# Optimization experiments

Hardware: AMD Instinct MI355X
Metric: run time of the kernel (lower is better)

Reference implementation:

```python
import jax, jax.numpy as jnp
import numpy as np

L, D, F, V = 24, 1024, 4096, 50277  # n_layer, n_embd, ffn hidden (4*D), vocab
RESCALE = 6


def _ln(x, w, b, eps=1e-5):
    m = jnp.mean(x, axis=-1, keepdims=True)
    v = jnp.mean(jnp.square(x - m), axis=-1, keepdims=True)
    return (x - m) * jax.lax.rsqrt(v + eps) * w + b


def setup_inputs() -> dict:
    key = jax.random.key(0)
    ks = iter(jax.random.split(key, 64))

    def nrm(shape, s=0.02):
        return jax.random.normal(next(ks), shape, jnp.float32) * s

    def uni(shape):
        return jax.random.uniform(next(ks), shape, jnp.float32)

    state = jnp.zeros((L, 5, D), jnp.float32).at[:, 4, :].set(-1e30)  # pp init
    return {
        "token_embd": jax.random.normal(next(ks), (D,), jnp.float32),
        "state": state,
        "emb_ln_w": jnp.ones((D,), jnp.float32),
        "emb_ln_b": jnp.zeros((D,), jnp.float32),
        "ln1_w": jnp.ones((L, D), jnp.float32),
        "ln1_b": jnp.zeros((L, D), jnp.float32),
        "ln2_w": jnp.ones((L, D), jnp.float32),
        "ln2_b": jnp.zeros((L, D), jnp.float32),
        "att_tmk": uni((L, D)),
        "att_tmv": uni((L, D)),
        "att_tmr": uni((L, D)),
        "att_tf": nrm((L, D), 0.5),
        "att_td": -jnp.exp(nrm((L, D), 0.5)),  # time_decay = -exp(w) at load
        "att_kw": nrm((L, D, D)),
        "att_vw": nrm((L, D, D)),
        "att_rw": nrm((L, D, D)),
        "att_ow": nrm((L, D, D)),
        "ffn_tmk": uni((L, D)),
        "ffn_tmr": uni((L, D)),
        "ffn_kw": nrm((L, F, D)),
        "ffn_vw": nrm((L, D, F)),
        "ffn_rw": nrm((L, D, D)),
        "out_ln_w": jnp.ones((D,), jnp.float32),
        "out_ln_b": jnp.zeros((D,), jnp.float32),
        "head_w": nrm((V, D)),
    }


def reference(token_embd, state, emb_ln_w, emb_ln_b, ln1_w, ln1_b, ln2_w, ln2_b,
              att_tmk, att_tmv, att_tmr, att_tf, att_td, att_kw, att_vw, att_rw,
              att_ow, ffn_tmk, ffn_tmr, ffn_kw, ffn_vw, ffn_rw,
              out_ln_w, out_ln_b, head_w):
    x0 = _ln(token_embd, emb_ln_w, emb_ln_b)  # encoder

    def layer(x, inputs):
        (i, st, l1w, l1b, l2w, l2b, tmk, tmv, tmr, tf, td,
         kw, vw, rw, ow, ftmk, ftmr, fkw, fvw, frw) = inputs
        # ---- time mixing ----
        xn = _ln(x, l1w, l1b)
        s_att, aa, bb, pp = st[1], st[2], st[3], st[4]
        xk = xn * tmk + s_att * (1 - tmk)
        xv = xn * tmv + s_att * (1 - tmv)
        xr = xn * tmr + s_att * (1 - tmr)
        r = jax.nn.sigmoid(rw @ xr)
        kk = kw @ xk
        vv = vw @ xv
        ww = tf + kk
        p = jnp.maximum(pp, ww)
        e1 = jnp.exp(pp - p)
        e2 = jnp.exp(ww - p)
        a = e1 * aa + e2 * vv
        b = e1 * bb + e2
        ww2 = pp + td
        p2 = jnp.maximum(ww2, kk)
        f1 = jnp.exp(ww2 - p2)
        f2 = jnp.exp(kk - p2)
        new_aa = f1 * aa + f2 * vv
        new_bb = f1 * bb + f2
        x = x + ow @ (r * (a / b))
        # ---- channel mixing ----
        xn2 = _ln(x, l2w, l2b)
        s_ffn = st[0]
        xk2 = xn2 * ftmk + s_ffn * (1 - ftmk)
        xr2 = xn2 * ftmr + s_ffn * (1 - ftmr)
        r2 = jax.nn.sigmoid(frw @ xr2)
        k2 = jnp.square(jax.nn.relu(fkw @ xk2))
        x = x + r2 * (fvw @ k2)
        # rescale every RESCALE layers
        x = jnp.where((i + 1) % RESCALE == 0, x * 0.5, x)
        new_st = jnp.stack([xn2, xn, new_aa, new_bb, p2])
        return x, new_st

    idx = jnp.arange(L)
    x, new_state = jax.lax.scan(
        layer, x0,
        (idx, state, ln1_w, ln1_b, ln2_w, ln2_b, att_tmk, att_tmv, att_tmr,
         att_tf, att_td, att_kw, att_vw, att_rw, att_ow, ffn_tmk, ffn_tmr,
         ffn_kw, ffn_vw, ffn_rw))
    logits = head_w @ _ln(x, out_ln_w, out_ln_b)  # decoder
    return logits, new_state
```

## Files before the change

### kernel.cpp

```cpp
#include <hip/hip_runtime.h>

#define DD 1024
#define FF 4096
#define LL 24
#define VV 50277


__device__ __forceinline__ float wave_sum(float v) {
#pragma unroll
    for (int o = 32; o > 0; o >>= 1) v += __shfl_xor(v, o, 64);
    return v;
}

__device__ __forceinline__ float block_sum(float v, float* scr) {
    v = wave_sum(v);
    int w = threadIdx.x >> 6;
    __syncthreads();
    if ((threadIdx.x & 63) == 0) scr[w] = v;
    __syncthreads();
    return scr[0] + scr[1] + scr[2] + scr[3];
}

__device__ __forceinline__ float4 ln_vec(float4 xv, const float* __restrict__ w,
                                         const float* __restrict__ b,
                                         float* scr, int t) {
    float s = xv.x + xv.y + xv.z + xv.w;
    float m = block_sum(s, scr) * (1.0f / (float)DD);
    float dx = xv.x - m, dy = xv.y - m, dz = xv.z - m, dw = xv.w - m;
    float var = block_sum(dx * dx + dy * dy + dz * dz + dw * dw, scr) * (1.0f / (float)DD);
    float rs = rsqrtf(var + 1e-5f);
    float4 w4 = ((const float4*)w)[t];
    float4 b4 = ((const float4*)b)[t];
    return make_float4(dx * rs * w4.x + b4.x, dy * rs * w4.y + b4.y,
                       dz * rs * w4.z + b4.z, dw * rs * w4.w + b4.w);
}


__global__ __launch_bounds__(256) void k_ln(const float* __restrict__ xin,
                                            const float* __restrict__ w,
                                            const float* __restrict__ b,
                                            float* __restrict__ xout) {
    __shared__ float scr[4];
    int t = threadIdx.x;
    float4 v = ((const float4*)xin)[t];
    float4 n = ln_vec(v, w, b, scr, t);
    ((float4*)xout)[t] = n;
}


__global__ __launch_bounds__(256) void k1_timemix(
    const float* __restrict__ x, const float* __restrict__ st,
    const float* __restrict__ l1w, const float* __restrict__ l1b,
    const float* __restrict__ tmk, const float* __restrict__ tmv,
    const float* __restrict__ tmr,
    const float* __restrict__ kw, const float* __restrict__ vw,
    const float* __restrict__ rw,
    float* __restrict__ kk, float* __restrict__ vv, float* __restrict__ rr,
    float* __restrict__ st_out) {
    __shared__ __align__(16) float xk[DD];
    __shared__ __align__(16) float xv_[DD];
    __shared__ __align__(16) float xr[DD];
    __shared__ float scr[4];
    int t = threadIdx.x;

    float4 xvec = ((const float4*)x)[t];
    float4 n = ln_vec(xvec, l1w, l1b, scr, t);
    if (blockIdx.x == 0) ((float4*)(st_out + DD))[t] = n;

    float4 sa = ((const float4*)(st + DD))[t];
    float4 mk = ((const float4*)tmk)[t];
    float4 mv = ((const float4*)tmv)[t];
    float4 mr = ((const float4*)tmr)[t];
    ((float4*)xk)[t] = make_float4(n.x * mk.x + sa.x * (1.f - mk.x),
                                   n.y * mk.y + sa.y * (1.f - mk.y),
                                   n.z * mk.z + sa.z * (1.f - mk.z),
                                   n.w * mk.w + sa.w * (1.f - mk.w));
    ((float4*)xv_)[t] = make_float4(n.x * mv.x + sa.x * (1.f - mv.x),
                                    n.y * mv.y + sa.y * (1.f - mv.y),
                                    n.z * mv.z + sa.z * (1.f - mv.z),
                                    n.w * mv.w + sa.w * (1.f - mv.w));
    ((float4*)xr)[t] = make_float4(n.x * mr.x + sa.x * (1.f - mr.x),
                                   n.y * mr.y + sa.y * (1.f - mr.y),
                                   n.z * mr.z + sa.z * (1.f - mr.z),
                                   n.w * mr.w + sa.w * (1.f - mr.w));
    __syncthreads();

    int lane = t & 63, w = t >> 6;
    int ridx = blockIdx.x * 4 + w;
    int m = ridx >> 10, row = ridx & 1023;
    const float* W = (m == 0 ? kw : (m == 1 ? vw : rw)) + (size_t)row * DD;
    const float* vec = (m == 0 ? xk : (m == 1 ? xv_ : xr));
    const float4* W4 = (const float4*)W;
    const float4* v4 = (const float4*)vec;
    float acc = 0.f;
#pragma unroll
    for (int j = 0; j < 4; ++j) {
        float4 a = W4[lane + 64 * j];
        float4 bx = v4[lane + 64 * j];
        acc = fmaf(a.x, bx.x, fmaf(a.y, bx.y, fmaf(a.z, bx.z, fmaf(a.w, bx.w, acc))));
    }
    acc = wave_sum(acc);
    if (lane == 0) {
        if (m == 0) kk[row] = acc;
        else if (m == 1) vv[row] = acc;
        else rr[row] = 1.0f / (1.0f + expf(-acc));
    }
}


__global__ __launch_bounds__(256) void k2_wkv_out(
    const float* __restrict__ st,
    const float* __restrict__ tf, const float* __restrict__ td,
    const float* __restrict__ kk, const float* __restrict__ vv,
    const float* __restrict__ rr, const float* __restrict__ ow,
    float* __restrict__ x, float* __restrict__ st_out) {
    __shared__ __align__(16) float rab[DD];
    int t = threadIdx.x;

    float4 kk4 = ((const float4*)kk)[t];
    float4 vv4 = ((const float4*)vv)[t];
    float4 r4  = ((const float4*)rr)[t];
    float4 aa4 = ((const float4*)(st + 2 * DD))[t];
    float4 bb4 = ((const float4*)(st + 3 * DD))[t];
    float4 pp4 = ((const float4*)(st + 4 * DD))[t];
    float4 tf4 = ((const float4*)tf)[t];
    float4 td4 = ((const float4*)td)[t];
    float4 rabv, naa, nbb, np2;
    const float* kkp = (const float*)&kk4; const float* vvp = (const float*)&vv4;
    const float* rp = (const float*)&r4;   const float* aap = (const float*)&aa4;
    const float* bbp = (const float*)&bb4; const float* ppp = (const float*)&pp4;
    const float* tfp = (const float*)&tf4; const float* tdp = (const float*)&td4;
#pragma unroll
    for (int c = 0; c < 4; ++c) {
        float kx = kkp[c], vx = vvp[c], rx = rp[c];
        float ax = aap[c], bx = bbp[c], px = ppp[c];
        float ww = tfp[c] + kx;
        float p = fmaxf(px, ww);
        float e1 = expf(px - p), e2 = expf(ww - p);
        float a = e1 * ax + e2 * vx;
        float b = e1 * bx + e2;
        ((float*)&rabv)[c] = rx * (a / b);
        float ww2 = px + tdp[c];
        float p2 = fmaxf(ww2, kx);
        float f1 = expf(ww2 - p2), f2 = expf(kx - p2);
        ((float*)&naa)[c] = f1 * ax + f2 * vx;
        ((float*)&nbb)[c] = f1 * bx + f2;
        ((float*)&np2)[c] = p2;
    }
    ((float4*)rab)[t] = rabv;
    if (blockIdx.x == 0) {
        ((float4*)(st_out + 2 * DD))[t] = naa;
        ((float4*)(st_out + 3 * DD))[t] = nbb;
        ((float4*)(st_out + 4 * DD))[t] = np2;
    }
    __syncthreads();

    int lane = t & 63, w = t >> 6;
    int row = blockIdx.x * 4 + w;
    const float4* W4 = (const float4*)(ow + (size_t)row * DD);
    const float4* v4 = (const float4*)rab;
    float acc = 0.f;
#pragma unroll
    for (int j = 0; j < 4; ++j) {
        float4 a = W4[lane + 64 * j];
        float4 bx = v4[lane + 64 * j];
        acc = fmaf(a.x, bx.x, fmaf(a.y, bx.y, fmaf(a.z, bx.z, fmaf(a.w, bx.w, acc))));
    }
    acc = wave_sum(acc);
    if (lane == 0) x[row] += acc;
}


__global__ __launch_bounds__(256) void k3_ffn_kr(
    const float* __restrict__ x, const float* __restrict__ st,
    const float* __restrict__ l2w, const float* __restrict__ l2b,
    const float* __restrict__ ftmk, const float* __restrict__ ftmr,
    const float* __restrict__ fkw, const float* __restrict__ frw,
    float* __restrict__ k2, float* __restrict__ r2, float* __restrict__ st_out) {
    __shared__ __align__(16) float xk2[DD];
    __shared__ __align__(16) float xr2[DD];
    __shared__ float scr[4];
    int t = threadIdx.x;

    float4 xvec = ((const float4*)x)[t];
    float4 n = ln_vec(xvec, l2w, l2b, scr, t);
    if (blockIdx.x == 0) ((float4*)st_out)[t] = n;

    float4 sf = ((const float4*)st)[t];
    float4 mk = ((const float4*)ftmk)[t];
    float4 mr = ((const float4*)ftmr)[t];
    ((float4*)xk2)[t] = make_float4(n.x * mk.x + sf.x * (1.f - mk.x),
                                    n.y * mk.y + sf.y * (1.f - mk.y),
                                    n.z * mk.z + sf.z * (1.f - mk.z),
                                    n.w * mk.w + sf.w * (1.f - mk.w));
    ((float4*)xr2)[t] = make_float4(n.x * mr.x + sf.x * (1.f - mr.x),
                                    n.y * mr.y + sf.y * (1.f - mr.y),
                                    n.z * mr.z + sf.z * (1.f - mr.z),
                                    n.w * mr.w + sf.w * (1.f - mr.w));
    __syncthreads();

    int lane = t & 63, w = t >> 6;
    int ridx = blockIdx.x * 4 + w;
    const float* W;
    const float* vec;
    if (ridx < FF) { W = fkw + (size_t)ridx * DD; vec = xk2; }
    else           { W = frw + (size_t)(ridx - FF) * DD; vec = xr2; }
    const float4* W4 = (const float4*)W;
    const float4* v4 = (const float4*)vec;
    float acc = 0.f;
#pragma unroll
    for (int j = 0; j < 4; ++j) {
        float4 a = W4[lane + 64 * j];
        float4 bx = v4[lane + 64 * j];
        acc = fmaf(a.x, bx.x, fmaf(a.y, bx.y, fmaf(a.z, bx.z, fmaf(a.w, bx.w, acc))));
    }
    acc = wave_sum(acc);
    if (lane == 0) {
        if (ridx < FF) {
            float rl = fmaxf(acc, 0.f);
            k2[ridx] = rl * rl;
        } else {
            r2[ridx - FF] = 1.0f / (1.0f + expf(-acc));
        }
    }
}


__global__ __launch_bounds__(256) void k4_ffn_v(
    const float* __restrict__ fvw, const float* __restrict__ k2,
    const float* __restrict__ r2, float* __restrict__ x, float scale) {
    __shared__ __align__(16) float k2s[FF];
    int t = threadIdx.x;
#pragma unroll
    for (int j = 0; j < 4; ++j)
        ((float4*)k2s)[t + 256 * j] = ((const float4*)k2)[t + 256 * j];
    __syncthreads();

    int lane = t & 63, w = t >> 6;
    int row = blockIdx.x * 4 + w;
    const float4* W4 = (const float4*)(fvw + (size_t)row * FF);
    const float4* v4 = (const float4*)k2s;
    float acc = 0.f;
#pragma unroll
    for (int j = 0; j < 16; ++j) {
        float4 a = W4[lane + 64 * j];
        float4 bx = v4[lane + 64 * j];
        acc = fmaf(a.x, bx.x, fmaf(a.y, bx.y, fmaf(a.z, bx.z, fmaf(a.w, bx.w, acc))));
    }
    acc = wave_sum(acc);
    if (lane == 0) x[row] = (x[row] + r2[row] * acc) * scale;
}


__global__ __launch_bounds__(256) void k_head(const float* __restrict__ head_w,
                                              const float* __restrict__ xn,
                                              float* __restrict__ logits) {
    __shared__ __align__(16) float xs[DD];
    int t = threadIdx.x;
    ((float4*)xs)[t] = ((const float4*)xn)[t];
    __syncthreads();

    int lane = t & 63, w = t >> 6;
    int row = blockIdx.x * 4 + w;
    if (row >= VV) return;
    const float4* W4 = (const float4*)(head_w + (size_t)row * DD);
    const float4* v4 = (const float4*)xs;
    float acc = 0.f;
#pragma unroll
    for (int j = 0; j < 4; ++j) {
        float4 a = W4[lane + 64 * j];
        float4 bx = v4[lane + 64 * j];
        acc = fmaf(a.x, bx.x, fmaf(a.y, bx.y, fmaf(a.z, bx.z, fmaf(a.w, bx.w, acc))));
    }
    acc = wave_sum(acc);
    if (lane == 0) logits[row] = acc;
}


extern "C" void kernel_launch(void* const* d_in, const int* in_sizes, int n_in,
                              void* d_out, int out_size, void* d_ws, size_t ws_size,
                              hipStream_t stream) {
    const float* token_embd = (const float*)d_in[0];
    const float* state      = (const float*)d_in[1];
    const float* emb_ln_w   = (const float*)d_in[2];
    const float* emb_ln_b   = (const float*)d_in[3];
    const float* ln1_w      = (const float*)d_in[4];
    const float* ln1_b      = (const float*)d_in[5];
    const float* ln2_w      = (const float*)d_in[6];
    const float* ln2_b      = (const float*)d_in[7];
    const float* att_tmk    = (const float*)d_in[8];
    const float* att_tmv    = (const float*)d_in[9];
    const float* att_tmr    = (const float*)d_in[10];
    const float* att_tf     = (const float*)d_in[11];
    const float* att_td     = (const float*)d_in[12];
    const float* att_kw     = (const float*)d_in[13];
    const float* att_vw     = (const float*)d_in[14];
    const float* att_rw     = (const float*)d_in[15];
    const float* att_ow     = (const float*)d_in[16];
    const float* ffn_tmk    = (const float*)d_in[17];
    const float* ffn_tmr    = (const float*)d_in[18];
    const float* ffn_kw     = (const float*)d_in[19];
    const float* ffn_vw     = (const float*)d_in[20];
    const float* ffn_rw     = (const float*)d_in[21];
    const float* out_ln_w   = (const float*)d_in[22];
    const float* out_ln_b   = (const float*)d_in[23];
    const float* head_w     = (const float*)d_in[24];

    float* logits = (float*)d_out;
    float* st_out_base = (float*)d_out + VV;

    float* ws  = (float*)d_ws;
    float* x   = ws;
    float* kk  = ws + 1024;
    float* vv  = ws + 2048;
    float* rr  = ws + 3072;
    float* k2  = ws + 4096;
    float* r2  = ws + 8192;
    float* xnH = ws + 9216;

    k_ln<<<1, 256, 0, stream>>>(token_embd, emb_ln_w, emb_ln_b, x);

    for (int i = 0; i < LL; ++i) {
        const float* st = state + (size_t)i * 5 * DD;
        float* sto = st_out_base + (size_t)i * 5 * DD;
        k1_timemix<<<768, 256, 0, stream>>>(
            x, st, ln1_w + i * DD, ln1_b + i * DD,
            att_tmk + i * DD, att_tmv + i * DD, att_tmr + i * DD,
            att_kw + (size_t)i * DD * DD, att_vw + (size_t)i * DD * DD,
            att_rw + (size_t)i * DD * DD, kk, vv, rr, sto);
        k2_wkv_out<<<256, 256, 0, stream>>>(
            st, att_tf + i * DD, att_td + i * DD, kk, vv, rr,
            att_ow + (size_t)i * DD * DD, x, sto);
        k3_ffn_kr<<<1280, 256, 0, stream>>>(
            x, st, ln2_w + i * DD, ln2_b + i * DD,
            ffn_tmk + i * DD, ffn_tmr + i * DD,
            ffn_kw + (size_t)i * FF * DD, ffn_rw + (size_t)i * DD * DD,
            k2, r2, sto);
        float scale = ((i + 1) % 6 == 0) ? 0.5f : 1.0f;
        k4_ffn_v<<<256, 256, 0, stream>>>(
            ffn_vw + (size_t)i * DD * FF, k2, r2, x, scale);
    }

    k_ln<<<1, 256, 0, stream>>>(x, out_ln_w, out_ln_b, xnH);
    k_head<<<(VV + 3) / 4, 256, 0, stream>>>(head_w, xnH, logits);
}
```

Baseline: 610.2 us.

## Prefetch upcoming layer weights into cache via extra blocks in each kernel

Each per-layer kernel gets PFB extra blocks that stream the weights needed by the next kernels (attention output, FFN key/value/receptance, next layer's k/v/r) through the cache, so that later GEMVs hit in cache (likely the large MI355X last-level cache) instead of HBM. The encoder layernorm is fused into the first time-mix kernel and the output layernorm into the head kernel, removing two single-block launches. Head rows are loaded before the layernorm to overlap latency. This relies on cache capacity and adds redundant memory traffic that competes with the current kernel's own loads.

```diff
diff --git a/kernel.cpp b/kernel.cpp
--- a/kernel.cpp
+++ b/kernel.cpp
@@ -4,6 +4,9 @@
 #define FF 4096
 #define LL 24
 #define VV 50277
+#define PFB 256
+
+typedef float v4f __attribute__((ext_vector_type(4)));
 
 
 __device__ __forceinline__ float wave_sum(float v) {
@@ -21,152 +24,150 @@
     return scr[0] + scr[1] + scr[2] + scr[3];
 }
 
-__device__ __forceinline__ float4 ln_vec(float4 xv, const float* __restrict__ w,
-                                         const float* __restrict__ b,
-                                         float* scr, int t) {
-    float s = xv.x + xv.y + xv.z + xv.w;
-    float m = block_sum(s, scr) * (1.0f / (float)DD);
-    float dx = xv.x - m, dy = xv.y - m, dz = xv.z - m, dw = xv.w - m;
-    float var = block_sum(dx * dx + dy * dy + dz * dz + dw * dw, scr) * (1.0f / (float)DD);
+__device__ __forceinline__ v4f ln_vec(v4f xv, const float* __restrict__ w,
+                                      const float* __restrict__ b, float* scr, int t) {
+    float m = block_sum(xv[0] + xv[1] + xv[2] + xv[3], scr) * (1.0f / 1024.0f);
+    v4f d = xv - m;
+    float var = block_sum(d[0]*d[0] + d[1]*d[1] + d[2]*d[2] + d[3]*d[3], scr) * (1.0f / 1024.0f);
     float rs = rsqrtf(var + 1e-5f);
-    float4 w4 = ((const float4*)w)[t];
-    float4 b4 = ((const float4*)b)[t];
-    return make_float4(dx * rs * w4.x + b4.x, dy * rs * w4.y + b4.y,
-                       dz * rs * w4.z + b4.z, dw * rs * w4.w + b4.w);
-}
-
-
-__global__ __launch_bounds__(256) void k_ln(const float* __restrict__ xin,
-                                            const float* __restrict__ w,
-                                            const float* __restrict__ b,
-                                            float* __restrict__ xout) {
-    __shared__ float scr[4];
-    int t = threadIdx.x;
-    float4 v = ((const float4*)xin)[t];
-    float4 n = ln_vec(v, w, b, scr, t);
-    ((float4*)xout)[t] = n;
+    v4f w4 = ((const v4f*)w)[t], b4 = ((const v4f*)b)[t];
+    return d * rs * w4 + b4;
+}
+
+__device__ __forceinline__ v4f mixv(v4f n, v4f s, v4f m) { return n * m + s * (1.0f - m); }
+
+__device__ __forceinline__ float dotv(v4f a, v4f x) {
+    return fmaf(a[0], x[0], fmaf(a[1], x[1], fmaf(a[2], x[2], a[3] * x[3])));
+}
+
+struct Row { v4f a, b, c, d; };
+
+__device__ __forceinline__ void row_load(Row& r, const float* p, int lane) {
+    const v4f* q = (const v4f*)p;
+    r.a = q[lane]; r.b = q[lane + 64]; r.c = q[lane + 128]; r.d = q[lane + 192];
+}
+__device__ __forceinline__ float row_dot(const Row& r, const v4f* v, int lane) {
+    return dotv(r.a, v[lane]) + dotv(r.b, v[lane + 64]) +
+           dotv(r.c, v[lane + 128]) + dotv(r.d, v[lane + 192]);
+}
+
+
+__device__ __forceinline__ void pf_region(const float* p, int nvec, int pb, int t) {
+    if (p == nullptr || nvec <= 0) return;
+    const v4f* q = (const v4f*)p;
+    int chunk = (nvec + PFB - 1) / PFB;
+    int lo = pb * chunk;
+    int end = lo + chunk; if (end > nvec) end = nvec;
+    int i = lo + t;
+    v4f a0 = {0,0,0,0}, a1 = a0, a2 = a0, a3 = a0, a4 = a0, a5 = a0, a6 = a0, a7 = a0;
+    for (; i + 1792 < end; i += 2048) {
+        v4f t0 = q[i],        t1 = q[i + 256],  t2 = q[i + 512],  t3 = q[i + 768];
+        v4f t4 = q[i + 1024], t5 = q[i + 1280], t6 = q[i + 1536], t7 = q[i + 1792];
+        a0 += t0; a1 += t1; a2 += t2; a3 += t3;
+        a4 += t4; a5 += t5; a6 += t6; a7 += t7;
+    }
+    for (; i < end; i += 256) a0 += q[i];
+    a0 = (a0 + a1) + (a2 + a3) + ((a4 + a5) + (a6 + a7));
+    asm volatile("" :: "v"(a0));
 }
 
 
 __global__ __launch_bounds__(256) void k1_timemix(
-    const float* __restrict__ x, const float* __restrict__ st,
+    const float* __restrict__ xin, const float* __restrict__ st,
+    const float* __restrict__ enc_w, const float* __restrict__ enc_b,
     const float* __restrict__ l1w, const float* __restrict__ l1b,
     const float* __restrict__ tmk, const float* __restrict__ tmv,
     const float* __restrict__ tmr,
     const float* __restrict__ kw, const float* __restrict__ vw,
     const float* __restrict__ rw,
     float* __restrict__ kk, float* __restrict__ vv, float* __restrict__ rr,
-    float* __restrict__ st_out) {
-    __shared__ __align__(16) float xk[DD];
-    __shared__ __align__(16) float xv_[DD];
-    __shared__ __align__(16) float xr[DD];
+    float* __restrict__ x0out, float* __restrict__ st_out,
+    const float* pfa, int na, const float* pfb, int nb) {
+    const int t = threadIdx.x;
+    int b = blockIdx.x;
+    if (b < PFB) { pf_region(pfa, na, b, t); pf_region(pfb, nb, b, t); return; }
+    b -= PFB;
+    __shared__ __align__(16) float s_k[DD], s_v[DD], s_r[DD];
     __shared__ float scr[4];
-    int t = threadIdx.x;
-
-    float4 xvec = ((const float4*)x)[t];
-    float4 n = ln_vec(xvec, l1w, l1b, scr, t);
-    if (blockIdx.x == 0) ((float4*)(st_out + DD))[t] = n;
-
-    float4 sa = ((const float4*)(st + DD))[t];
-    float4 mk = ((const float4*)tmk)[t];
-    float4 mv = ((const float4*)tmv)[t];
-    float4 mr = ((const float4*)tmr)[t];
-    ((float4*)xk)[t] = make_float4(n.x * mk.x + sa.x * (1.f - mk.x),
-                                   n.y * mk.y + sa.y * (1.f - mk.y),
-                                   n.z * mk.z + sa.z * (1.f - mk.z),
-                                   n.w * mk.w + sa.w * (1.f - mk.w));
-    ((float4*)xv_)[t] = make_float4(n.x * mv.x + sa.x * (1.f - mv.x),
-                                    n.y * mv.y + sa.y * (1.f - mv.y),
-                                    n.z * mv.z + sa.z * (1.f - mv.z),
-                                    n.w * mv.w + sa.w * (1.f - mv.w));
-    ((float4*)xr)[t] = make_float4(n.x * mr.x + sa.x * (1.f - mr.x),
-                                   n.y * mr.y + sa.y * (1.f - mr.y),
-                                   n.z * mr.z + sa.z * (1.f - mr.z),
-                                   n.w * mr.w + sa.w * (1.f - mr.w));
-    __syncthreads();
-
-    int lane = t & 63, w = t >> 6;
-    int ridx = blockIdx.x * 4 + w;
-    int m = ridx >> 10, row = ridx & 1023;
-    const float* W = (m == 0 ? kw : (m == 1 ? vw : rw)) + (size_t)row * DD;
-    const float* vec = (m == 0 ? xk : (m == 1 ? xv_ : xr));
-    const float4* W4 = (const float4*)W;
-    const float4* v4 = (const float4*)vec;
-    float acc = 0.f;
-#pragma unroll
-    for (int j = 0; j < 4; ++j) {
-        float4 a = W4[lane + 64 * j];
-        float4 bx = v4[lane + 64 * j];
-        acc = fmaf(a.x, bx.x, fmaf(a.y, bx.y, fmaf(a.z, bx.z, fmaf(a.w, bx.w, acc))));
-    }
-    acc = wave_sum(acc);
+    const int lane = t & 63, w = t >> 6;
+
+    v4f xv = ((const v4f*)xin)[t];
+    if (enc_w) xv = ln_vec(xv, enc_w, enc_b, scr, t);
+    if (x0out && b == 0) ((v4f*)x0out)[t] = xv;
+    v4f n = ln_vec(xv, l1w, l1b, scr, t);
+    if (b == 0) ((v4f*)(st_out + DD))[t] = n;
+    {
+        v4f sa = ((const v4f*)(st + DD))[t];
+        ((v4f*)s_k)[t] = mixv(n, sa, ((const v4f*)tmk)[t]);
+        ((v4f*)s_v)[t] = mixv(n, sa, ((const v4f*)tmv)[t]);
+        ((v4f*)s_r)[t] = mixv(n, sa, ((const v4f*)tmr)[t]);
+    }
+    __syncthreads();
+
+    const int ridx = b * 4 + w, m = ridx >> 10, row = ridx & 1023;
+    Row W;
+    row_load(W, (m == 0 ? kw : m == 1 ? vw : rw) + (size_t)row * DD, lane);
+    const v4f* vec = (const v4f*)(m == 0 ? s_k : m == 1 ? s_v : s_r);
+    float acc = wave_sum(row_dot(W, vec, lane));
     if (lane == 0) {
-        if (m == 0) kk[row] = acc;
+        if (m == 0)      kk[row] = acc;
         else if (m == 1) vv[row] = acc;
-        else rr[row] = 1.0f / (1.0f + expf(-acc));
+        else             rr[row] = 1.0f / (1.0f + expf(-acc));
     }
 }
 
 
 __global__ __launch_bounds__(256) void k2_wkv_out(
-    const float* __restrict__ st,
-    const float* __restrict__ tf, const float* __restrict__ td,
+    const float* __restrict__ st, const float* __restrict__ tf,
+    const float* __restrict__ td,
     const float* __restrict__ kk, const float* __restrict__ vv,
     const float* __restrict__ rr, const float* __restrict__ ow,
-    float* __restrict__ x, float* __restrict__ st_out) {
+    float* __restrict__ x, float* __restrict__ st_out,
+    const float* pfa, int na, const float* pfb, int nb) {
+    const int t = threadIdx.x;
+    int b = blockIdx.x;
+    if (b < PFB) { pf_region(pfa, na, b, t); pf_region(pfb, nb, b, t); return; }
+    b -= PFB;
     __shared__ __align__(16) float rab[DD];
-    int t = threadIdx.x;
-
-    float4 kk4 = ((const float4*)kk)[t];
-    float4 vv4 = ((const float4*)vv)[t];
-    float4 r4  = ((const float4*)rr)[t];
-    float4 aa4 = ((const float4*)(st + 2 * DD))[t];
-    float4 bb4 = ((const float4*)(st + 3 * DD))[t];
-    float4 pp4 = ((const float4*)(st + 4 * DD))[t];
-    float4 tf4 = ((const float4*)tf)[t];
-    float4 td4 = ((const float4*)td)[t];
-    float4 rabv, naa, nbb, np2;
-    const float* kkp = (const float*)&kk4; const float* vvp = (const float*)&vv4;
-    const float* rp = (const float*)&r4;   const float* aap = (const float*)&aa4;
-    const float* bbp = (const float*)&bb4; const float* ppp = (const float*)&pp4;
-    const float* tfp = (const float*)&tf4; const float* tdp = (const float*)&td4;
+    const int lane = t & 63, w = t >> 6;
+
+    {
+        v4f kx = ((const v4f*)kk)[t];
+        v4f vx = ((const v4f*)vv)[t];
+        v4f rx = ((const v4f*)rr)[t];
+        v4f aa = ((const v4f*)(st + 2 * DD))[t];
+        v4f bb = ((const v4f*)(st + 3 * DD))[t];
+        v4f pp = ((const v4f*)(st + 4 * DD))[t];
+        v4f tf4 = ((const v4f*)tf)[t];
+        v4f td4 = ((const v4f*)td)[t];
+        v4f rb, naa, nbb, np2;
 #pragma unroll
-    for (int c = 0; c < 4; ++c) {
-        float kx = kkp[c], vx = vvp[c], rx = rp[c];
-        float ax = aap[c], bx = bbp[c], px = ppp[c];
-        float ww = tfp[c] + kx;
-        float p = fmaxf(px, ww);
-        float e1 = expf(px - p), e2 = expf(ww - p);
-        float a = e1 * ax + e2 * vx;
-        float b = e1 * bx + e2;
-        ((float*)&rabv)[c] = rx * (a / b);
-        float ww2 = px + tdp[c];
-        float p2 = fmaxf(ww2, kx);
-        float f1 = expf(ww2 - p2), f2 = expf(kx - p2);
-        ((float*)&naa)[c] = f1 * ax + f2 * vx;
-        ((float*)&nbb)[c] = f1 * bx + f2;
-        ((float*)&np2)[c] = p2;
-    }
-    ((float4*)rab)[t] = rabv;
-    if (blockIdx.x == 0) {
-        ((float4*)(st_out + 2 * DD))[t] = naa;
-        ((float4*)(st_out + 3 * DD))[t] = nbb;
-        ((float4*)(st_out + 4 * DD))[t] = np2;
-    }
-    __syncthreads();
-
-    int lane = t & 63, w = t >> 6;
-    int row = blockIdx.x * 4 + w;
-    const float4* W4 = (const float4*)(ow + (size_t)row * DD);
-    const float4* v4 = (const float4*)rab;
-    float acc = 0.f;
-#pragma unroll
-    for (int j = 0; j < 4; ++j) {
-        float4 a = W4[lane + 64 * j];
-        float4 bx = v4[lane + 64 * j];
-        acc = fmaf(a.x, bx.x, fmaf(a.y, bx.y, fmaf(a.z, bx.z, fmaf(a.w, bx.w, acc))));
-    }
-    acc = wave_sum(acc);
+        for (int c = 0; c < 4; ++c) {
+            float kc = kx[c], vc = vx[c];
+            float wwc = tf4[c] + kc;
+            float p = fmaxf(pp[c], wwc);
+            float e1 = expf(pp[c] - p), e2 = expf(wwc - p);
+            rb[c] = rx[c] * ((e1 * aa[c] + e2 * vc) / (e1 * bb[c] + e2));
+            float ww2 = pp[c] + td4[c];
+            float p2 = fmaxf(ww2, kc);
+            float f1 = expf(ww2 - p2), f2 = expf(kc - p2);
+            naa[c] = f1 * aa[c] + f2 * vc;
+            nbb[c] = f1 * bb[c] + f2;
+            np2[c] = p2;
+        }
+        ((v4f*)rab)[t] = rb;
+        if (b == 0) {
+            ((v4f*)(st_out + 2 * DD))[t] = naa;
+            ((v4f*)(st_out + 3 * DD))[t] = nbb;
+            ((v4f*)(st_out + 4 * DD))[t] = np2;
+        }
+    }
+    __syncthreads();
+
+    const int row = b * 4 + w;
+    Row W;
+    row_load(W, ow + (size_t)row * DD, lane);
+    float acc = wave_sum(row_dot(W, (const v4f*)rab, lane));
     if (lane == 0) x[row] += acc;
 }
 
@@ -176,76 +177,65 @@
     const float* __restrict__ l2w, const float* __restrict__ l2b,
     const float* __restrict__ ftmk, const float* __restrict__ ftmr,
     const float* __restrict__ fkw, const float* __restrict__ frw,
-    float* __restrict__ k2, float* __restrict__ r2, float* __restrict__ st_out) {
-    __shared__ __align__(16) float xk2[DD];
-    __shared__ __align__(16) float xr2[DD];
+    float* __restrict__ k2, float* __restrict__ r2, float* __restrict__ st_out,
+    const float* pfa, int na, const float* pfb, int nb) {
+    const int t = threadIdx.x;
+    int b = blockIdx.x;
+    if (b < PFB) { pf_region(pfa, na, b, t); pf_region(pfb, nb, b, t); return; }
+    b -= PFB;
+    __shared__ __align__(16) float s_k[DD], s_r[DD];
     __shared__ float scr[4];
-    int t = threadIdx.x;
-
-    float4 xvec = ((const float4*)x)[t];
-    float4 n = ln_vec(xvec, l2w, l2b, scr, t);
-    if (blockIdx.x == 0) ((float4*)st_out)[t] = n;
-
-    float4 sf = ((const float4*)st)[t];
-    float4 mk = ((const float4*)ftmk)[t];
-    float4 mr = ((const float4*)ftmr)[t];
-    ((float4*)xk2)[t] = make_float4(n.x * mk.x + sf.x * (1.f - mk.x),
-                                    n.y * mk.y + sf.y * (1.f - mk.y),
-                                    n.z * mk.z + sf.z * (1.f - mk.z),
-                                    n.w * mk.w + sf.w * (1.f - mk.w));
-    ((float4*)xr2)[t] = make_float4(n.x * mr.x + sf.x * (1.f - mr.x),
-                                    n.y * mr.y + sf.y * (1.f - mr.y),
-                                    n.z * mr.z + sf.z * (1.f - mr.z),
-                                    n.w * mr.w + sf.w * (1.f - mr.w));
-    __syncthreads();
-
-    int lane = t & 63, w = t >> 6;
-    int ridx = blockIdx.x * 4 + w;
-    const float* W;
-    const float* vec;
-    if (ridx < FF) { W = fkw + (size_t)ridx * DD; vec = xk2; }
-    else           { W = frw + (size_t)(ridx - FF) * DD; vec = xr2; }
-    const float4* W4 = (const float4*)W;
-    const float4* v4 = (const float4*)vec;
-    float acc = 0.f;
-#pragma unroll
-    for (int j = 0; j < 4; ++j) {
-        float4 a = W4[lane + 64 * j];
-        float4 bx = v4[lane + 64 * j];
-        acc = fmaf(a.x, bx.x, fmaf(a.y, bx.y, fmaf(a.z, bx.z, fmaf(a.w, bx.w, acc))));
-    }
-    acc = wave_sum(acc);
+    const int lane = t & 63, w = t >> 6;
+
+    v4f xv = ((const v4f*)x)[t];
+    v4f n = ln_vec(xv, l2w, l2b, scr, t);
+    if (b == 0) ((v4f*)st_out)[t] = n;
+    {
+        v4f sf = ((const v4f*)st)[t];
+        ((v4f*)s_k)[t] = mixv(n, sf, ((const v4f*)ftmk)[t]);
+        ((v4f*)s_r)[t] = mixv(n, sf, ((const v4f*)ftmr)[t]);
+    }
+    __syncthreads();
+
+    const int ridx = b * 4 + w;
+    const float* Wp;
+    const v4f* vec;
+    if (ridx < FF) { Wp = fkw + (size_t)ridx * DD; vec = (const v4f*)s_k; }
+    else           { Wp = frw + (size_t)(ridx - FF) * DD; vec = (const v4f*)s_r; }
+    Row W;
+    row_load(W, Wp, lane);
+    float acc = wave_sum(row_dot(W, vec, lane));
     if (lane == 0) {
-        if (ridx < FF) {
-            float rl = fmaxf(acc, 0.f);
-            k2[ridx] = rl * rl;
-        } else {
-            r2[ridx - FF] = 1.0f / (1.0f + expf(-acc));
-        }
+        if (ridx < FF) { float rl = fmaxf(acc, 0.f); k2[ridx] = rl * rl; }
+        else           r2[ridx - FF] = 1.0f / (1.0f + expf(-acc));
     }
 }
 
 
 __global__ __launch_bounds__(256) void k4_ffn_v(
     const float* __restrict__ fvw, const float* __restrict__ k2,
-    const float* __restrict__ r2, float* __restrict__ x, float scale) {
+    const float* __restrict__ r2, float* __restrict__ x, float scale,
+    const float* pfa, int na, const float* pfb, int nb) {
+    const int t = threadIdx.x;
+    int b = blockIdx.x;
+    if (b < PFB) { pf_region(pfa, na, b, t); pf_region(pfb, nb, b, t); return; }
+    b -= PFB;
     __shared__ __align__(16) float k2s[FF];
-    int t = threadIdx.x;
+    const int lane = t & 63, w = t >> 6;
 #pragma unroll
     for (int j = 0; j < 4; ++j)
-        ((float4*)k2s)[t + 256 * j] = ((const float4*)k2)[t + 256 * j];
-    __syncthreads();
-
-    int lane = t & 63, w = t >> 6;
-    int row = blockIdx.x * 4 + w;
-    const float4* W4 = (const float4*)(fvw + (size_t)row * FF);
-    const float4* v4 = (const float4*)k2s;
+        ((v4f*)k2s)[t + 256 * j] = ((const v4f*)k2)[t + 256 * j];
+    __syncthreads();
+
+    const int row = b * 4 + w;
+    const v4f* W4 = (const v4f*)(fvw + (size_t)row * FF);
+    const v4f* v4 = (const v4f*)k2s;
     float acc = 0.f;
 #pragma unroll
     for (int j = 0; j < 16; ++j) {
-        float4 a = W4[lane + 64 * j];
-        float4 bx = v4[lane + 64 * j];
-        acc = fmaf(a.x, bx.x, fmaf(a.y, bx.y, fmaf(a.z, bx.z, fmaf(a.w, bx.w, acc))));
+        v4f a = W4[lane + 64 * j];
+        v4f bx = v4[lane + 64 * j];
+        acc = fmaf(a[0], bx[0], fmaf(a[1], bx[1], fmaf(a[2], bx[2], fmaf(a[3], bx[3], acc))));
     }
     acc = wave_sum(acc);
     if (lane == 0) x[row] = (x[row] + r2[row] * acc) * scale;
@@ -253,27 +243,24 @@
 
 
 __global__ __launch_bounds__(256) void k_head(const float* __restrict__ head_w,
-                                              const float* __restrict__ xn,
+                                              const float* __restrict__ x,
+                                              const float* __restrict__ olw,
+                                              const float* __restrict__ olb,
                                               float* __restrict__ logits) {
     __shared__ __align__(16) float xs[DD];
-    int t = threadIdx.x;
-    ((float4*)xs)[t] = ((const float4*)xn)[t];
-    __syncthreads();
-
-    int lane = t & 63, w = t >> 6;
-    int row = blockIdx.x * 4 + w;
-    if (row >= VV) return;
-    const float4* W4 = (const float4*)(head_w + (size_t)row * DD);
-    const float4* v4 = (const float4*)xs;
-    float acc = 0.f;
-#pragma unroll
-    for (int j = 0; j < 4; ++j) {
-        float4 a = W4[lane + 64 * j];
-        float4 bx = v4[lane + 64 * j];
-        acc = fmaf(a.x, bx.x, fmaf(a.y, bx.y, fmaf(a.z, bx.z, fmaf(a.w, bx.w, acc))));
-    }
-    acc = wave_sum(acc);
-    if (lane == 0) logits[row] = acc;
+    __shared__ float scr[4];
+    const int t = threadIdx.x, lane = t & 63, w = t >> 6;
+    const int row = blockIdx.x * 4 + w;
+    Row W;
+    if (row < VV) row_load(W, head_w + (size_t)row * DD, lane);
+    v4f xv = ((const v4f*)x)[t];
+    v4f nx = ln_vec(xv, olw, olb, scr, t);
+    ((v4f*)xs)[t] = nx;
+    __syncthreads();
+    if (row < VV) {
+        float acc = wave_sum(row_dot(W, (const v4f*)xs, lane));
+        if (lane == 0) logits[row] = acc;
+    }
 }
 
 
@@ -314,33 +301,50 @@
     float* kk  = ws + 1024;
     float* vv  = ws + 2048;
     float* rr  = ws + 3072;
-    float* k2  = ws + 4096;
-    float* r2  = ws + 8192;
-    float* xnH = ws + 9216;
-
-    k_ln<<<1, 256, 0, stream>>>(token_embd, emb_ln_w, emb_ln_b, x);
+    float* k2b = ws + 4096;
+    float* r2b = ws + 8192;
+
+    const int V_D   = DD * DD / 4;
+    const int V_FKH = FF * DD / 8;
 
     for (int i = 0; i < LL; ++i) {
         const float* st = state + (size_t)i * 5 * DD;
         float* sto = st_out_base + (size_t)i * 5 * DD;
-        k1_timemix<<<768, 256, 0, stream>>>(
-            x, st, ln1_w + i * DD, ln1_b + i * DD,
+        const float* kw_i  = att_kw + (size_t)i * DD * DD;
+        const float* vw_i  = att_vw + (size_t)i * DD * DD;
+        const float* rw_i  = att_rw + (size_t)i * DD * DD;
+        const float* ow_i  = att_ow + (size_t)i * DD * DD;
+        const float* fkw_i = ffn_kw + (size_t)i * FF * DD;
+        const float* fvw_i = ffn_vw + (size_t)i * DD * FF;
+        const float* frw_i = ffn_rw + (size_t)i * DD * DD;
+        const bool last = (i == LL - 1);
+
+        k1_timemix<<<PFB + 768, 256, 0, stream>>>(
+            (i == 0) ? token_embd : x, st,
+            (i == 0) ? emb_ln_w : nullptr, (i == 0) ? emb_ln_b : nullptr,
+            ln1_w + i * DD, ln1_b + i * DD,
             att_tmk + i * DD, att_tmv + i * DD, att_tmr + i * DD,
-            att_kw + (size_t)i * DD * DD, att_vw + (size_t)i * DD * DD,
-            att_rw + (size_t)i * DD * DD, kk, vv, rr, sto);
-        k2_wkv_out<<<256, 256, 0, stream>>>(
-            st, att_tf + i * DD, att_td + i * DD, kk, vv, rr,
-            att_ow + (size_t)i * DD * DD, x, sto);
-        k3_ffn_kr<<<1280, 256, 0, stream>>>(
+            kw_i, vw_i, rw_i, kk, vv, rr,
+            (i == 0) ? x : nullptr, sto,
+            ow_i, V_D, fkw_i, V_FKH);
+
+        k2_wkv_out<<<PFB + 256, 256, 0, stream>>>(
+            st, att_tf + i * DD, att_td + i * DD, kk, vv, rr, ow_i, x, sto,
+            fkw_i + (size_t)FF * DD / 2, V_FKH, frw_i, V_D);
+
+        k3_ffn_kr<<<PFB + 1280, 256, 0, stream>>>(
             x, st, ln2_w + i * DD, ln2_b + i * DD,
-            ffn_tmk + i * DD, ffn_tmr + i * DD,
-            ffn_kw + (size_t)i * FF * DD, ffn_rw + (size_t)i * DD * DD,
-            k2, r2, sto);
+            ffn_tmk + i * DD, ffn_tmr + i * DD, fkw_i, frw_i,
+            k2b, r2b, sto,
+            fvw_i, 2 * V_FKH,
+            last ? nullptr : rw_i + DD * DD, last ? 0 : V_D);
+
         float scale = ((i + 1) % 6 == 0) ? 0.5f : 1.0f;
-        k4_ffn_v<<<256, 256, 0, stream>>>(
-            ffn_vw + (size_t)i * DD * FF, k2, r2, x, scale);
-    }
-
-    k_ln<<<1, 256, 0, stream>>>(x, out_ln_w, out_ln_b, xnH);
-    k_head<<<(VV + 3) / 4, 256, 0, stream>>>(head_w, xnH, logits);
-}
+        k4_ffn_v<<<PFB + 256, 256, 0, stream>>>(
+            fvw_i, k2b, r2b, x, scale,
+            last ? nullptr : kw_i + DD * DD, last ? 0 : V_D,
+            last ? nullptr : vw_i + DD * DD, last ? 0 : V_D);
+    }
+
+    k_head<<<(VV + 3) / 4, 256, 0, stream>>>(head_w, x, out_ln_w, out_ln_b, logits);
+}
```

Measured after the change: 722.5 us. 1.18x slower.
